# Optimization experiments

Hardware: AMD Instinct MI355X
Metric: run time of the kernel (lower is better)

The kernel has to match this reference:

```python
import jax, jax.numpy as jnp
import numpy as np

KS = 3          # kernel_size
PAD = 1         # padding
STRIDE = 1      # stride
INC = 32
OUTC = 64
N = KS * KS     # number of sampling points


def conv2d(x, w, b, stride, pad):
    out = jax.lax.conv_general_dilated(
        x, w, (stride, stride), [(pad, pad), (pad, pad)],
        dimension_numbers=('NCHW', 'OIHW', 'NCHW'))
    return out if b is None else out + b[None, :, None, None]


def setup_inputs() -> dict:
    key = jax.random.key(0)
    k = jax.random.split(key, 5)
    x = jax.random.normal(k[0], (2, INC, 192, 192), jnp.float32)
    # main conv: kernel=ks, stride=ks, bias=None in the original
    conv_w = jax.random.normal(k[1], (OUTC, INC, KS, KS), jnp.float32) * (1.0 / np.sqrt(INC * KS * KS))
    # p_conv: weight init to 0 in the original (output = bias broadcast); unused in the math
    p_conv_w = jnp.zeros((2 * N, INC, 3, 3), jnp.float32)
    p_conv_b = jax.random.uniform(k[2], (2 * N,), jnp.float32, minval=-0.05, maxval=0.05)
    # p_conv1: produces scalar scale map A; keep it near 1 for realistic sampling
    p1_w = jax.random.normal(k[3], (1, INC, 3, 3), jnp.float32) * 0.05
    p1_b = jax.random.uniform(k[4], (1,), jnp.float32, minval=0.9, maxval=1.1)
    return {'x': x, 'conv_w': conv_w, 'p_conv_w': p_conv_w, 'p_conv_b': p_conv_b,
            'p1_w': p1_w, 'p1_b': p1_b}


def _gather_xq(xp, qx, qy, Wp):
    # xp: (b,c,Hp,Wp); qx,qy: (b,h,w,N) int -> (b,c,h,w,N)
    b, c = xp.shape[0], xp.shape[1]
    xf = xp.reshape(b, c, -1)
    idx = qx * Wp + qy  # linear index into flattened padded map (matches torch gather)
    def per_b(xf_b, idx_b):
        return xf_b[:, idx_b.ravel()].reshape((c,) + idx_b.shape)
    return jax.vmap(per_b)(xf, idx)


def _forward(x, conv_w, p_conv_w, p_conv_b, p1_w, p1_b):
    dt = x.dtype
    offset = conv2d(x, p_conv_w, p_conv_b, STRIDE, 1)   # (b,2N,h,w) -- shape-only in original
    A = conv2d(x, p1_w, p1_b, STRIDE, 1)                # (b,1,h,w) scale map
    h, w = offset.shape[2], offset.shape[3]
    xp = jnp.pad(x, ((0, 0), (0, 0), (PAD, PAD), (PAD, PAD)))
    Hp, Wp = xp.shape[2], xp.shape[3]

    # p_n: kernel-relative grid offsets, shape (1,2N,1,1)
    rng = jnp.arange(-(KS - 1) // 2, (KS - 1) // 2 + 1)
    pnx, pny = jnp.meshgrid(rng, rng, indexing='ij')
    p_n = jnp.concatenate([pnx.ravel(), pny.ravel()]).astype(dt).reshape(1, 2 * N, 1, 1)
    # p_0: absolute center coords starting at 1 (accounts for zero padding)
    gx, gy = jnp.meshgrid(jnp.arange(1, h * STRIDE + 1, STRIDE),
                          jnp.arange(1, w * STRIDE + 1, STRIDE), indexing='ij')
    p_0 = jnp.concatenate([jnp.tile(gx[None], (N, 1, 1)),
                           jnp.tile(gy[None], (N, 1, 1))], 0)[None].astype(dt)

    p = p_0 + A * p_n                       # (b,2N,h,w): scaled sampling grid
    p = jnp.transpose(p, (0, 2, 3, 1))      # (b,h,w,2N)

    q_lt = jnp.floor(p)
    q_rb = q_lt + 1
    qx_lt = jnp.clip(q_lt[..., :N], 0, Hp - 1).astype(jnp.int32)
    qy_lt = jnp.clip(q_lt[..., N:], 0, Wp - 1).astype(jnp.int32)
    qx_rb = jnp.clip(q_rb[..., :N], 0, Hp - 1).astype(jnp.int32)
    qy_rb = jnp.clip(q_rb[..., N:], 0, Wp - 1).astype(jnp.int32)

    px = jnp.clip(p[..., :N], 0, Hp - 1)
    py = jnp.clip(p[..., N:], 0, Wp - 1)

    fx_lt, fy_lt = qx_lt.astype(dt), qy_lt.astype(dt)
    fx_rb, fy_rb = qx_rb.astype(dt), qy_rb.astype(dt)
    g_lt = (1 + (fx_lt - px)) * (1 + (fy_lt - py))
    g_rb = (1 - (fx_rb - px)) * (1 - (fy_rb - py))
    g_lb = (1 + (fx_lt - px)) * (1 - (fy_rb - py))   # q_lb = (x_lt, y_rb)
    g_rt = (1 - (fx_rb - px)) * (1 + (fy_lt - py))   # q_rt = (x_rb, y_lt)

    x_lt = _gather_xq(xp, qx_lt, qy_lt, Wp)
    x_rb = _gather_xq(xp, qx_rb, qy_rb, Wp)
    x_lb = _gather_xq(xp, qx_lt, qy_rb, Wp)
    x_rt = _gather_xq(xp, qx_rb, qy_lt, Wp)

    # bilinear combine -> (b,c,h,w,N)
    x_offset = (g_lt[:, None] * x_lt + g_rb[:, None] * x_rb
                + g_lb[:, None] * x_lb + g_rt[:, None] * x_rt)

    # the ks-stride conv over the reshaped [h*ks, w*ks] map is exactly a
    # contraction over (c, n) with n = ki*ks + kj (same ordering as p_n flatten)
    wk = conv_w.reshape(conv_w.shape[0], conv_w.shape[1], N)
    out = jnp.einsum('ocn,bchwn->bohw', wk, x_offset)
    return out


def reference(x, conv_w, p_conv_w, p_conv_b, p1_w, p1_b):
    return _forward(x, conv_w, p_conv_w, p_conv_b, p1_w, p1_b)
```

## Files before the change

### kernel.cpp

```cpp
#include <hip/hip_runtime.h>

typedef __attribute__((ext_vector_type(4))) float f32x4;
typedef __attribute__((ext_vector_type(4))) int   i32x4;
typedef __attribute__((ext_vector_type(8))) short s16x8;

__device__ __forceinline__ unsigned short f2bf(float f) {
  union { float f; unsigned u; } v; v.f = f;
  unsigned r = v.u + 0x7fffu + ((v.u >> 16) & 1u);
  return (unsigned short)(r >> 16);
}

__device__ __forceinline__ void add8(i32x4 v, float g, f32x4& s0, f32x4& s1) {
  union { int ii; float ff; } u;
  u.ii = v[0] << 16;                  s0[0] = fmaf(g, u.ff, s0[0]);
  u.ii = v[0] & (int)0xffff0000u;     s0[1] = fmaf(g, u.ff, s0[1]);
  u.ii = v[1] << 16;                  s0[2] = fmaf(g, u.ff, s0[2]);
  u.ii = v[1] & (int)0xffff0000u;     s0[3] = fmaf(g, u.ff, s0[3]);
  u.ii = v[2] << 16;                  s1[0] = fmaf(g, u.ff, s1[0]);
  u.ii = v[2] & (int)0xffff0000u;     s1[1] = fmaf(g, u.ff, s1[1]);
  u.ii = v[3] << 16;                  s1[2] = fmaf(g, u.ff, s1[2]);
  u.ii = v[3] & (int)0xffff0000u;     s1[3] = fmaf(g, u.ff, s1[3]);
}

__global__ __launch_bounds__(256) void k_prep(const float* __restrict__ x,
                                              unsigned short* __restrict__ xp) {
  int t = blockIdx.x * 256 + threadIdx.x;
  if (t >= 2 * 194 * 194 * 4) return;
  int pix = t >> 2, c8 = t & 3;
  int b = pix / (194 * 194);
  int r = pix % (194 * 194);
  int i = r / 194 - 1, j = r % 194 - 1;
  bool ok = ((unsigned)i < 192u) && ((unsigned)j < 192u);
  const float* src = x + (size_t)b * 32 * 36864 + (size_t)(c8 * 8) * 36864 + i * 192 + j;
  unsigned v[8];
  #pragma unroll
  for (int k = 0; k < 8; k++) v[k] = ok ? (unsigned)f2bf(src[k * 36864]) : 0u;
  i32x4 pv;
  pv[0] = (int)(v[0] | (v[1] << 16));
  pv[1] = (int)(v[2] | (v[3] << 16));
  pv[2] = (int)(v[4] | (v[5] << 16));
  pv[3] = (int)(v[6] | (v[7] << 16));
  *(i32x4*)(xp + (size_t)pix * 32 + c8 * 8) = pv;
}

__global__ __launch_bounds__(256) void k_wfrag(const float* __restrict__ w,
                                               short* __restrict__ wf) {
  int t = blockIdx.x * 256 + threadIdx.x;
  if (t >= 9 * 4 * 64) return;
  int n = t / 256;
  int ot = (t / 64) % 4;
  int lane = t % 64;
  int o = ot * 16 + (lane & 15);
  int cb = (lane >> 4) * 8;
  #pragma unroll
  for (int jj = 0; jj < 8; jj++) {
    float v = w[(o * 32 + cb + jj) * 9 + n];
    wf[(size_t)t * 8 + jj] = (short)f2bf(v);
  }
}

__global__ __launch_bounds__(256) void k_main(const unsigned short* __restrict__ xp,
                                              const float* __restrict__ p1w,
                                              const float* __restrict__ p1b,
                                              const s16x8* __restrict__ wfv,
                                              float* __restrict__ out) {
  __shared__ float wlds[288];
  for (int idx = threadIdx.x; idx < 288; idx += 256) {
    int c = idx / 9, tap = idx % 9;
    wlds[tap * 32 + c] = p1w[idx];
  }
  __syncthreads();

  int lane = threadIdx.x & 63;
  int bs = (blockIdx.x & 7) * 144 + (blockIdx.x >> 3);
  int W = bs * 4 + (threadIdx.x >> 6);
  int b = W / 2304;
  int r = W % 2304;
  int i = r / 12;
  int j0 = (r % 12) * 16;
  int m = lane & 15, quad = lane >> 4;
  int j = j0 + m;
  const unsigned short* xpb = xp + (size_t)b * (194 * 194 * 32) + quad * 8;

  float a = 0.f;
  #pragma unroll
  for (int tap = 0; tap < 9; tap++) {
    int kh = tap / 3, kw = tap % 3;
    i32x4 v = *(const i32x4*)(xpb + ((i + kh) * 194 + (j + kw)) * 32);
    const f32x4* wp = (const f32x4*)(wlds + tap * 32 + quad * 8);
    f32x4 w0 = wp[0], w1 = wp[1];
    union { int ii; float ff; } u;
    u.ii = v[0] << 16;              a = fmaf(u.ff, w0[0], a);
    u.ii = v[0] & (int)0xffff0000u; a = fmaf(u.ff, w0[1], a);
    u.ii = v[1] << 16;              a = fmaf(u.ff, w0[2], a);
    u.ii = v[1] & (int)0xffff0000u; a = fmaf(u.ff, w0[3], a);
    u.ii = v[2] << 16;              a = fmaf(u.ff, w1[0], a);
    u.ii = v[2] & (int)0xffff0000u; a = fmaf(u.ff, w1[1], a);
    u.ii = v[3] << 16;              a = fmaf(u.ff, w1[2], a);
    u.ii = v[3] & (int)0xffff0000u; a = fmaf(u.ff, w1[3], a);
  }
  a += __shfl_xor(a, 16);
  a += __shfl_xor(a, 32);
  float A = a + p1b[0];

  f32x4 acc0 = {0.f, 0.f, 0.f, 0.f};
  f32x4 acc1 = acc0, acc2 = acc0, acc3 = acc0;
  float cx = (float)(i + 1), cy = (float)(j + 1);
  int icx = i + 1, icy = j + 1;

  #pragma unroll
  for (int n = 0; n < 9; n++) {
    const int dx = n / 3 - 1, dy = n % 3 - 1;
    f32x4 s0 = {0.f, 0.f, 0.f, 0.f}, s1 = s0;
    if (dx == 0 && dy == 0) {
      i32x4 v = *(const i32x4*)(xpb + (icx * 194 + icy) * 32);
      add8(v, 1.0f, s0, s1);
    } else if (dy == 0) {
      float px = cx + A * (float)dx;
      float flx = floorf(px);
      float qlx = fminf(fmaxf(flx, 0.f), 193.f);
      float qrx = fminf(fmaxf(flx + 1.f, 0.f), 193.f);
      float pxc = fminf(fmaxf(px, 0.f), 193.f);
      float gxl = 1.f + (qlx - pxc), gxr = 1.f - (qrx - pxc);
      i32x4 vl = *(const i32x4*)(xpb + ((int)qlx * 194 + icy) * 32);
      i32x4 vr = *(const i32x4*)(xpb + ((int)qrx * 194 + icy) * 32);
      add8(vl, gxl, s0, s1);
      add8(vr, gxr, s0, s1);
    } else if (dx == 0) {
      float py = cy + A * (float)dy;
      float fly = floorf(py);
      float qly = fminf(fmaxf(fly, 0.f), 193.f);
      float qry = fminf(fmaxf(fly + 1.f, 0.f), 193.f);
      float pyc = fminf(fmaxf(py, 0.f), 193.f);
      float gyl = 1.f + (qly - pyc), gyr = 1.f - (qry - pyc);
      i32x4 vl = *(const i32x4*)(xpb + (icx * 194 + (int)qly) * 32);
      i32x4 vr = *(const i32x4*)(xpb + (icx * 194 + (int)qry) * 32);
      add8(vl, gyl, s0, s1);
      add8(vr, gyr, s0, s1);
    } else {
      float px = cx + A * (float)dx;
      float py = cy + A * (float)dy;
      float flx = floorf(px), fly = floorf(py);
      float qlx = fminf(fmaxf(flx, 0.f), 193.f);
      float qly = fminf(fmaxf(fly, 0.f), 193.f);
      float qrx = fminf(fmaxf(flx + 1.f, 0.f), 193.f);
      float qry = fminf(fmaxf(fly + 1.f, 0.f), 193.f);
      float pxc = fminf(fmaxf(px, 0.f), 193.f);
      float pyc = fminf(fmaxf(py, 0.f), 193.f);
      float gxl = 1.f + (qlx - pxc), gxr = 1.f - (qrx - pxc);
      float gyl = 1.f + (qly - pyc), gyr = 1.f - (qry - pyc);
      int ixl = (int)qlx, iyl = (int)qly, ixr = (int)qrx, iyr = (int)qry;
      i32x4 vlt = *(const i32x4*)(xpb + (ixl * 194 + iyl) * 32);
      i32x4 vrb = *(const i32x4*)(xpb + (ixr * 194 + iyr) * 32);
      i32x4 vlb = *(const i32x4*)(xpb + (ixl * 194 + iyr) * 32);
      i32x4 vrt = *(const i32x4*)(xpb + (ixr * 194 + iyl) * 32);
      add8(vlt, gxl * gyl, s0, s1);
      add8(vrb, gxr * gyr, s0, s1);
      add8(vlb, gxl * gyr, s0, s1);
      add8(vrt, gxr * gyl, s0, s1);
    }
    s16x8 af;
    af[0] = (short)f2bf(s0[0]); af[1] = (short)f2bf(s0[1]);
    af[2] = (short)f2bf(s0[2]); af[3] = (short)f2bf(s0[3]);
    af[4] = (short)f2bf(s1[0]); af[5] = (short)f2bf(s1[1]);
    af[6] = (short)f2bf(s1[2]); af[7] = (short)f2bf(s1[3]);
    int wb = n * 256 + lane;
    acc0 = __builtin_amdgcn_mfma_f32_16x16x32_bf16(af, wfv[wb],       acc0, 0, 0, 0);
    acc1 = __builtin_amdgcn_mfma_f32_16x16x32_bf16(af, wfv[wb + 64],  acc1, 0, 0, 0);
    acc2 = __builtin_amdgcn_mfma_f32_16x16x32_bf16(af, wfv[wb + 128], acc2, 0, 0, 0);
    acc3 = __builtin_amdgcn_mfma_f32_16x16x32_bf16(af, wfv[wb + 192], acc3, 0, 0, 0);
  }

  int o0 = lane & 15;
  int jout = j0 + quad * 4;
  float* op = out + (size_t)b * 64 * 36864 + (size_t)o0 * 36864 + i * 192 + jout;
  *(f32x4*)(op) = acc0;
  *(f32x4*)(op + 16 * 36864) = acc1;
  *(f32x4*)(op + 32 * 36864) = acc2;
  *(f32x4*)(op + 48 * 36864) = acc3;
}

extern "C" void kernel_launch(void* const* d_in, const int* in_sizes, int n_in,
                              void* d_out, int out_size, void* d_ws, size_t ws_size,
                              hipStream_t stream) {
  const float* x      = (const float*)d_in[0];
  const float* conv_w = (const float*)d_in[1];
  const float* p1w    = (const float*)d_in[4];
  const float* p1b    = (const float*)d_in[5];
  float* out = (float*)d_out;

  unsigned short* xp = (unsigned short*)d_ws;
  short* wf = (short*)(xp + 2 * 194 * 194 * 32);

  k_prep<<<(2 * 194 * 194 * 4 + 255) / 256, 256, 0, stream>>>(x, xp);
  k_wfrag<<<9, 256, 0, stream>>>(conv_w, wf);
  k_main<<<1152, 256, 0, stream>>>(xp, p1w, p1b, (const s16x8*)wf, out);
}
```

Baseline: 100.4 us.

## Batch bilinear gathers ahead of MFMA, reuse center tap, fuse prep kernels

Computes all sampling offsets and weights up front, then issues the gathered loads for several taps in batches before the bilinear-combine and MFMA steps, so memory latency overlaps compute. The center tap reuses the value already loaded for the scale-map convolution instead of loading it again. Packing to bf16 now uses a perm-based round-half-up, which replaces round-to-nearest-even. The weight-fragment kernel is merged into the prep kernel, saving one launch. Holding the batched loads raises register pressure and may lower occupancy.

```diff
diff --git a/kernel.cpp b/kernel.cpp
--- a/kernel.cpp
+++ b/kernel.cpp
@@ -4,10 +4,15 @@
 typedef __attribute__((ext_vector_type(4))) int   i32x4;
 typedef __attribute__((ext_vector_type(8))) short s16x8;
 
-__device__ __forceinline__ unsigned short f2bf(float f) {
+__device__ __forceinline__ unsigned short f2bf_rn(float f) {
   union { float f; unsigned u; } v; v.f = f;
   unsigned r = v.u + 0x7fffu + ((v.u >> 16) & 1u);
   return (unsigned short)(r >> 16);
+}
+
+__device__ __forceinline__ int packbf2(float lo, float hi) {
+  union { float f; unsigned u; } a, b; a.f = lo; b.f = hi;
+  return (int)__builtin_amdgcn_perm(b.u + 0x8000u, a.u + 0x8000u, 0x07060302u);
 }
 
 __device__ __forceinline__ void add8(i32x4 v, float g, f32x4& s0, f32x4& s1) {
@@ -22,40 +27,50 @@
   u.ii = v[3] & (int)0xffff0000u;     s1[3] = fmaf(g, u.ff, s1[3]);
 }
 
+__device__ __forceinline__ void axis_cw(float p, int& il, int& ir, float& gl, float& gr) {
+  float fl = floorf(p);
+  float ql = fminf(fmaxf(fl, 0.f), 193.f);
+  float qr = fminf(fmaxf(fl + 1.f, 0.f), 193.f);
+  float pc = fminf(fmaxf(p, 0.f), 193.f);
+  gl = 1.f + (ql - pc);
+  gr = 1.f - (qr - pc);
+  il = (int)ql; ir = (int)qr;
+}
+
 __global__ __launch_bounds__(256) void k_prep(const float* __restrict__ x,
-                                              unsigned short* __restrict__ xp) {
+                                              unsigned short* __restrict__ xp,
+                                              const float* __restrict__ w,
+                                              short* __restrict__ wf) {
   int t = blockIdx.x * 256 + threadIdx.x;
-  if (t >= 2 * 194 * 194 * 4) return;
-  int pix = t >> 2, c8 = t & 3;
-  int b = pix / (194 * 194);
-  int r = pix % (194 * 194);
-  int i = r / 194 - 1, j = r % 194 - 1;
-  bool ok = ((unsigned)i < 192u) && ((unsigned)j < 192u);
-  const float* src = x + (size_t)b * 32 * 36864 + (size_t)(c8 * 8) * 36864 + i * 192 + j;
-  unsigned v[8];
-  #pragma unroll
-  for (int k = 0; k < 8; k++) v[k] = ok ? (unsigned)f2bf(src[k * 36864]) : 0u;
-  i32x4 pv;
-  pv[0] = (int)(v[0] | (v[1] << 16));
-  pv[1] = (int)(v[2] | (v[3] << 16));
-  pv[2] = (int)(v[4] | (v[5] << 16));
-  pv[3] = (int)(v[6] | (v[7] << 16));
-  *(i32x4*)(xp + (size_t)pix * 32 + c8 * 8) = pv;
-}
-
-__global__ __launch_bounds__(256) void k_wfrag(const float* __restrict__ w,
-                                               short* __restrict__ wf) {
-  int t = blockIdx.x * 256 + threadIdx.x;
-  if (t >= 9 * 4 * 64) return;
-  int n = t / 256;
-  int ot = (t / 64) % 4;
-  int lane = t % 64;
-  int o = ot * 16 + (lane & 15);
-  int cb = (lane >> 4) * 8;
-  #pragma unroll
-  for (int jj = 0; jj < 8; jj++) {
-    float v = w[(o * 32 + cb + jj) * 9 + n];
-    wf[(size_t)t * 8 + jj] = (short)f2bf(v);
+  if (t < 2 * 194 * 194 * 4) {
+    int pix = t >> 2, c8 = t & 3;
+    int b = pix / (194 * 194);
+    int r = pix % (194 * 194);
+    int i = r / 194 - 1, j = r % 194 - 1;
+    bool ok = ((unsigned)i < 192u) && ((unsigned)j < 192u);
+    const float* src = x + (size_t)b * 32 * 36864 + (size_t)(c8 * 8) * 36864 + i * 192 + j;
+    unsigned v[8];
+    #pragma unroll
+    for (int k = 0; k < 8; k++) v[k] = ok ? (unsigned)f2bf_rn(src[k * 36864]) : 0u;
+    i32x4 pv;
+    pv[0] = (int)(v[0] | (v[1] << 16));
+    pv[1] = (int)(v[2] | (v[3] << 16));
+    pv[2] = (int)(v[4] | (v[5] << 16));
+    pv[3] = (int)(v[6] | (v[7] << 16));
+    *(i32x4*)(xp + (size_t)pix * 32 + c8 * 8) = pv;
+  } else {
+    int u = t - 2 * 194 * 194 * 4;
+    if (u >= 9 * 4 * 64) return;
+    int n = u / 256;
+    int ot = (u / 64) % 4;
+    int lane = u % 64;
+    int o = ot * 16 + (lane & 15);
+    int cb = (lane >> 4) * 8;
+    #pragma unroll
+    for (int jj = 0; jj < 8; jj++) {
+      float v = w[(o * 32 + cb + jj) * 9 + n];
+      wf[(size_t)u * 8 + jj] = (short)f2bf_rn(v);
+    }
   }
 }
 
@@ -83,10 +98,12 @@
   const unsigned short* xpb = xp + (size_t)b * (194 * 194 * 32) + quad * 8;
 
   float a = 0.f;
+  i32x4 vcen;
   #pragma unroll
   for (int tap = 0; tap < 9; tap++) {
     int kh = tap / 3, kw = tap % 3;
     i32x4 v = *(const i32x4*)(xpb + ((i + kh) * 194 + (j + kw)) * 32);
+    if (tap == 4) vcen = v;
     const f32x4* wp = (const f32x4*)(wlds + tap * 32 + quad * 8);
     f32x4 w0 = wp[0], w1 = wp[1];
     union { int ii; float ff; } u;
@@ -103,73 +120,74 @@
   a += __shfl_xor(a, 32);
   float A = a + p1b[0];
 
-  f32x4 acc0 = {0.f, 0.f, 0.f, 0.f};
-  f32x4 acc1 = acc0, acc2 = acc0, acc3 = acc0;
   float cx = (float)(i + 1), cy = (float)(j + 1);
   int icx = i + 1, icy = j + 1;
-
+  int offs[9][4];
+  float gws[9][4];
   #pragma unroll
   for (int n = 0; n < 9; n++) {
     const int dx = n / 3 - 1, dy = n % 3 - 1;
-    f32x4 s0 = {0.f, 0.f, 0.f, 0.f}, s1 = s0;
-    if (dx == 0 && dy == 0) {
-      i32x4 v = *(const i32x4*)(xpb + (icx * 194 + icy) * 32);
-      add8(v, 1.0f, s0, s1);
-    } else if (dy == 0) {
-      float px = cx + A * (float)dx;
-      float flx = floorf(px);
-      float qlx = fminf(fmaxf(flx, 0.f), 193.f);
-      float qrx = fminf(fmaxf(flx + 1.f, 0.f), 193.f);
-      float pxc = fminf(fmaxf(px, 0.f), 193.f);
-      float gxl = 1.f + (qlx - pxc), gxr = 1.f - (qrx - pxc);
-      i32x4 vl = *(const i32x4*)(xpb + ((int)qlx * 194 + icy) * 32);
-      i32x4 vr = *(const i32x4*)(xpb + ((int)qrx * 194 + icy) * 32);
-      add8(vl, gxl, s0, s1);
-      add8(vr, gxr, s0, s1);
+    if (dx == 0 && dy == 0) continue;
+    if (dy == 0) {
+      int il, ir; float gl, gr;
+      axis_cw(cx + A * (float)dx, il, ir, gl, gr);
+      offs[n][0] = (il * 194 + icy) * 32; gws[n][0] = gl;
+      offs[n][1] = (ir * 194 + icy) * 32; gws[n][1] = gr;
     } else if (dx == 0) {
-      float py = cy + A * (float)dy;
-      float fly = floorf(py);
-      float qly = fminf(fmaxf(fly, 0.f), 193.f);
-      float qry = fminf(fmaxf(fly + 1.f, 0.f), 193.f);
-      float pyc = fminf(fmaxf(py, 0.f), 193.f);
-      float gyl = 1.f + (qly - pyc), gyr = 1.f - (qry - pyc);
-      i32x4 vl = *(const i32x4*)(xpb + (icx * 194 + (int)qly) * 32);
-      i32x4 vr = *(const i32x4*)(xpb + (icx * 194 + (int)qry) * 32);
-      add8(vl, gyl, s0, s1);
-      add8(vr, gyr, s0, s1);
+      int il, ir; float gl, gr;
+      axis_cw(cy + A * (float)dy, il, ir, gl, gr);
+      offs[n][0] = (icx * 194 + il) * 32; gws[n][0] = gl;
+      offs[n][1] = (icx * 194 + ir) * 32; gws[n][1] = gr;
     } else {
-      float px = cx + A * (float)dx;
-      float py = cy + A * (float)dy;
-      float flx = floorf(px), fly = floorf(py);
-      float qlx = fminf(fmaxf(flx, 0.f), 193.f);
-      float qly = fminf(fmaxf(fly, 0.f), 193.f);
-      float qrx = fminf(fmaxf(flx + 1.f, 0.f), 193.f);
-      float qry = fminf(fmaxf(fly + 1.f, 0.f), 193.f);
-      float pxc = fminf(fmaxf(px, 0.f), 193.f);
-      float pyc = fminf(fmaxf(py, 0.f), 193.f);
-      float gxl = 1.f + (qlx - pxc), gxr = 1.f - (qrx - pxc);
-      float gyl = 1.f + (qly - pyc), gyr = 1.f - (qry - pyc);
-      int ixl = (int)qlx, iyl = (int)qly, ixr = (int)qrx, iyr = (int)qry;
-      i32x4 vlt = *(const i32x4*)(xpb + (ixl * 194 + iyl) * 32);
-      i32x4 vrb = *(const i32x4*)(xpb + (ixr * 194 + iyr) * 32);
-      i32x4 vlb = *(const i32x4*)(xpb + (ixl * 194 + iyr) * 32);
-      i32x4 vrt = *(const i32x4*)(xpb + (ixr * 194 + iyl) * 32);
-      add8(vlt, gxl * gyl, s0, s1);
-      add8(vrb, gxr * gyr, s0, s1);
-      add8(vlb, gxl * gyr, s0, s1);
-      add8(vrt, gxr * gyl, s0, s1);
+      int ilx, irx, ily, iry; float gxl, gxr, gyl, gyr;
+      axis_cw(cx + A * (float)dx, ilx, irx, gxl, gxr);
+      axis_cw(cy + A * (float)dy, ily, iry, gyl, gyr);
+      offs[n][0] = (ilx * 194 + ily) * 32; gws[n][0] = gxl * gyl;
+      offs[n][1] = (irx * 194 + iry) * 32; gws[n][1] = gxr * gyr;
+      offs[n][2] = (ilx * 194 + iry) * 32; gws[n][2] = gxl * gyr;
+      offs[n][3] = (irx * 194 + ily) * 32; gws[n][3] = gxr * gyl;
     }
-    s16x8 af;
-    af[0] = (short)f2bf(s0[0]); af[1] = (short)f2bf(s0[1]);
-    af[2] = (short)f2bf(s0[2]); af[3] = (short)f2bf(s0[3]);
-    af[4] = (short)f2bf(s1[0]); af[5] = (short)f2bf(s1[1]);
-    af[6] = (short)f2bf(s1[2]); af[7] = (short)f2bf(s1[3]);
-    int wb = n * 256 + lane;
+  }
+
+  const int cnt[9] = {4, 2, 4, 2, 0, 2, 4, 2, 4};
+  i32x4 dat[9][4];
+  f32x4 acc0 = {0.f, 0.f, 0.f, 0.f};
+  f32x4 acc1 = acc0, acc2 = acc0, acc3 = acc0;
+
+#define LOAD_STEP(n)                                                      \
+  { _Pragma("unroll") for (int c = 0; c < 4; c++)                         \
+      if (c < cnt[n]) dat[n][c] = *(const i32x4*)(xpb + offs[n][c]); }
+
+#define PROC_STEP(n)                                                      \
+  { f32x4 s0 = {0.f, 0.f, 0.f, 0.f}, s1 = s0;                             \
+    _Pragma("unroll") for (int c = 0; c < 4; c++)                         \
+      if (c < cnt[n]) add8(dat[n][c], gws[n][c], s0, s1);                 \
+    s16x8 af; int* ai = (int*)&af;                                        \
+    ai[0] = packbf2(s0[0], s0[1]); ai[1] = packbf2(s0[2], s0[3]);         \
+    ai[2] = packbf2(s1[0], s1[1]); ai[3] = packbf2(s1[2], s1[3]);         \
+    int wb = (n) * 256 + lane;                                            \
+    acc0 = __builtin_amdgcn_mfma_f32_16x16x32_bf16(af, wfv[wb],       acc0, 0, 0, 0); \
+    acc1 = __builtin_amdgcn_mfma_f32_16x16x32_bf16(af, wfv[wb + 64],  acc1, 0, 0, 0); \
+    acc2 = __builtin_amdgcn_mfma_f32_16x16x32_bf16(af, wfv[wb + 128], acc2, 0, 0, 0); \
+    acc3 = __builtin_amdgcn_mfma_f32_16x16x32_bf16(af, wfv[wb + 192], acc3, 0, 0, 0); }
+
+  LOAD_STEP(0) LOAD_STEP(1) LOAD_STEP(2)
+  LOAD_STEP(3) LOAD_STEP(5)
+  PROC_STEP(0) PROC_STEP(1) PROC_STEP(2)
+  LOAD_STEP(6) LOAD_STEP(7) LOAD_STEP(8)
+  {
+    s16x8 af; int* ai = (int*)&af;
+    ai[0] = vcen[0]; ai[1] = vcen[1]; ai[2] = vcen[2]; ai[3] = vcen[3];
+    int wb = 4 * 256 + lane;
     acc0 = __builtin_amdgcn_mfma_f32_16x16x32_bf16(af, wfv[wb],       acc0, 0, 0, 0);
     acc1 = __builtin_amdgcn_mfma_f32_16x16x32_bf16(af, wfv[wb + 64],  acc1, 0, 0, 0);
     acc2 = __builtin_amdgcn_mfma_f32_16x16x32_bf16(af, wfv[wb + 128], acc2, 0, 0, 0);
     acc3 = __builtin_amdgcn_mfma_f32_16x16x32_bf16(af, wfv[wb + 192], acc3, 0, 0, 0);
   }
+  PROC_STEP(3) PROC_STEP(5)
+  PROC_STEP(6) PROC_STEP(7) PROC_STEP(8)
+#undef LOAD_STEP
+#undef PROC_STEP
 
   int o0 = lane & 15;
   int jout = j0 + quad * 4;
@@ -192,7 +210,7 @@
   unsigned short* xp = (unsigned short*)d_ws;
   short* wf = (short*)(xp + 2 * 194 * 194 * 32);
 
-  k_prep<<<(2 * 194 * 194 * 4 + 255) / 256, 256, 0, stream>>>(x, xp);
-  k_wfrag<<<9, 256, 0, stream>>>(conv_w, wf);
+  int prep_threads = 2 * 194 * 194 * 4 + 9 * 4 * 64;
+  k_prep<<<(prep_threads + 255) / 256, 256, 0, stream>>>(x, xp, conv_w, wf);
   k_main<<<1152, 256, 0, stream>>>(xp, p1w, p1b, (const s16x8*)wf, out);
 }
```

After: 97.83 us. 1.03x faster.
